# Kernel tuning notes

Measured on AMD Instinct MI355X. Metric: run time of the kernel, lower is better.

## Reference

```python
import jax, jax.numpy as jnp
import numpy as np

D_MODEL = 768
NUM_HEADS = 12
D_K = D_MODEL // NUM_HEADS
WINDOW = 16
SPARSITY = 0.8
NEG = -1e9


def _pos_encoding(seq_len, d_model, dtype):
    pos = jnp.arange(seq_len, dtype=jnp.float32)[:, None]
    div = jnp.exp(jnp.arange(0, d_model, 2, dtype=jnp.float32) * (-np.log(10000.0) / d_model))
    pe = jnp.zeros((seq_len, d_model), dtype=jnp.float32)
    pe = pe.at[:, 0::2].set(jnp.sin(pos * div))
    pe = pe.at[:, 1::2].set(jnp.cos(pos * div))
    return pe.astype(dtype)


def _layernorm(x, gamma, beta, eps=1e-5):
    mu = jnp.mean(x, axis=-1, keepdims=True)
    var = jnp.mean(jnp.square(x - mu), axis=-1, keepdims=True)
    return (x - mu) * jax.lax.rsqrt(var + eps) * gamma + beta


def _split_heads(x):  # [B,S,D] -> [B,H,S,dk]
    b, s, _ = x.shape
    return x.reshape(b, s, NUM_HEADS, D_K).transpose(0, 2, 1, 3)


def _attn(q, k, v, mask):  # mask broadcastable to [B,H,S,S], bool
    scores = jnp.einsum('bhqd,bhkd->bhqk', q, k) / jnp.sqrt(jnp.asarray(D_K, q.dtype))
    scores = jnp.where(mask, scores, jnp.asarray(NEG, q.dtype))
    w = jax.nn.softmax(scores, axis=-1)
    out = jnp.einsum('bhqk,bhkd->bhqd', w, v)
    b, h, s, d = out.shape
    return out.transpose(0, 2, 1, 3).reshape(b, s, h * d)


def setup_inputs() -> dict:
    key = jax.random.key(0)
    ks = jax.random.split(key, 16)
    d = D_MODEL
    sc = 1.0 / np.sqrt(d)
    inp = {
        'x': jax.random.normal(ks[0], (2, 2048, d), jnp.float32),
        'wgq': jax.random.normal(ks[1], (d, d), jnp.float32) * sc,
        'wgk': jax.random.normal(ks[2], (d, d), jnp.float32) * sc,
        'wgv': jax.random.normal(ks[3], (d, d), jnp.float32) * sc,
        'wlq': jax.random.normal(ks[4], (d, d), jnp.float32) * sc,
        'wlk': jax.random.normal(ks[5], (d, d), jnp.float32) * sc,
        'wlv': jax.random.normal(ks[6], (d, d), jnp.float32) * sc,
        'wtq': jax.random.normal(ks[7], (d, d), jnp.float32) * sc,
        'wtk': jax.random.normal(ks[8], (d, d), jnp.float32) * sc,
        'wtv': jax.random.normal(ks[9], (d, d), jnp.float32) * sc,
        'w_out': jax.random.normal(ks[10], (3 * d, d), jnp.float32) * (1.0 / np.sqrt(3 * d)),
        'b_out': jnp.zeros((d,), jnp.float32),
        'w_gate': jax.random.normal(ks[11], (d, 3), jnp.float32) * sc,
        'b_gate': jnp.zeros((3,), jnp.float32),
        'w_sparse': jax.random.normal(ks[12], (d, 1), jnp.float32) * sc,
        'b_sparse': jnp.zeros((1,), jnp.float32),
        'g_gamma': jnp.ones((d,), jnp.float32), 'g_beta': jnp.zeros((d,), jnp.float32),
        'l_gamma': jnp.ones((d,), jnp.float32), 'l_beta': jnp.zeros((d,), jnp.float32),
        't_gamma': jnp.ones((d,), jnp.float32), 't_beta': jnp.zeros((d,), jnp.float32),
    }
    return inp


def reference(x, wgq, wgk, wgv, wlq, wlk, wlv, wtq, wtk, wtv,
              w_out, b_out, w_gate, b_gate, w_sparse, b_sparse,
              g_gamma, g_beta, l_gamma, l_beta, t_gamma, t_beta):
    b, s, d = x.shape
    # positional encoding branch input (dropout is identity at eval)
    x_pos = x + _pos_encoding(s, d, x.dtype)[None]

    # focus gate over mean-pooled tokens -> [B,3]
    fw = jax.nn.softmax(x.mean(axis=1) @ w_gate + b_gate, axis=-1)
    gw, lw, tw = fw[:, 0, None, None], fw[:, 1, None, None], fw[:, 2, None, None]

    # sparse (global) mask: keep top-k important columns per batch
    importance = (x @ w_sparse + b_sparse)[..., 0]  # [B,S]
    k = max(1, int((1.0 - SPARSITY) * s))
    _, topk_idx = jax.lax.top_k(importance, k)
    sparse = jnp.zeros((b, s), bool).at[jnp.arange(b)[:, None], topk_idx].set(True)
    sparse_mask = sparse[:, None, None, :]  # [B,1,1,S]

    idx = jnp.arange(s)
    rel = idx[None, :] - idx[:, None]
    half = WINDOW // 2
    local_mask = ((rel >= -half) & (rel <= half))[None, None]  # [1,1,S,S]

    stride = max(1, s // 8)
    temporal_cols = (idx % stride) == 0
    temporal_mask = jnp.broadcast_to(temporal_cols[None, :], (s, s))[None, None]

    # global branch
    g = _attn(_split_heads(x @ wgq), _split_heads(x @ wgk), _split_heads(x @ wgv), sparse_mask)
    g = _layernorm(g, g_gamma, g_beta)
    # local branch
    l = _attn(_split_heads(x @ wlq), _split_heads(x @ wlk), _split_heads(x @ wlv), local_mask)
    l = _layernorm(l, l_gamma, l_beta)
    # temporal branch (uses pos-encoded input)
    t = _attn(_split_heads(x_pos @ wtq), _split_heads(x_pos @ wtk), _split_heads(x_pos @ wtv), temporal_mask)
    t = _layernorm(t, t_gamma, t_beta)

    combined = jnp.concatenate([g * gw, l * lw, t * tw], axis=-1)
    return combined @ w_out + b_out
```

## Files before the change

### kernel.cpp

```cpp
#include <hip/hip_runtime.h>
#include <cstdint>

constexpr int BB   = 2;
constexpr int SS   = 2048;
constexpr int DD   = 768;
constexpr int HH   = 12;
constexpr int NTOK = BB * SS;
constexpr int KSEL = 409;
constexpr int KPAD = 448;
constexpr int NKT  = 7;

typedef __bf16 bf16x8 __attribute__((ext_vector_type(8)));
typedef float  f32x4  __attribute__((ext_vector_type(4)));

__device__ __forceinline__ float b2f(unsigned short u) {
  return __uint_as_float(((unsigned)u) << 16);
}
__device__ __forceinline__ unsigned short f2b(float f) {
  unsigned u = __float_as_uint(f);
  u += 0x7fffu + ((u >> 16) & 1u);
  return (unsigned short)(u >> 16);
}
__device__ __forceinline__ unsigned long long shfl_xor_u64(unsigned long long v, int m) {
  unsigned lo = (unsigned)v, hi = (unsigned)(v >> 32);
  lo = __shfl_xor(lo, m, 64);
  hi = __shfl_xor(hi, m, 64);
  return ((unsigned long long)hi << 32) | lo;
}

__device__ __forceinline__ void gload_lds16(const void* gsrc, void* ldst) {
  __builtin_amdgcn_global_load_lds(
      (__attribute__((address_space(1))) void*)(gsrc),
      (__attribute__((address_space(3))) void*)(ldst), 16, 0, 0);
}

__global__ __launch_bounds__(256) void mega_pre(
    const float* __restrict__ x, const float* __restrict__ wsp,
    const float* __restrict__ bsp,
    unsigned short* __restrict__ xb, unsigned short* __restrict__ xpb,
    float* __restrict__ imp,
    const float* w0, const float* w1, const float* w2, const float* w3,
    const float* w4, const float* w5, const float* w6, const float* w7,
    const float* w8, const float* w9,
    unsigned short* __restrict__ WTx4, unsigned short* __restrict__ WTkv,
    unsigned short* __restrict__ WTqt, unsigned short* __restrict__ WTtkv,
    unsigned short* __restrict__ WTo,
    float* __restrict__ partial) {
  __shared__ float tile[32][33];
  int id = blockIdx.x;
  int tid = threadIdx.x;

  if (id < SS) {
    int srow = id;
    const float* xr0 = x + (long)srow * DD;
    const float* xr1 = x + (long)(SS + srow) * DD;
    float acc0 = 0.f, acc1 = 0.f;
#pragma unroll
    for (int k = 0; k < 3; ++k) {
      int c = tid + k * 256;
      int j2 = c & ~1;
      float freq = __expf((float)j2 * -0.011992630692677323f);
      float ang = (float)srow * freq;
      float pe = (c & 1) ? cosf(ang) : sinf(ang);
      float w = wsp[c];
      float x0 = xr0[c], x1 = xr1[c];
      xb[(long)srow * DD + c]        = f2b(x0);
      xb[(long)(SS + srow) * DD + c] = f2b(x1);
      xpb[(long)srow * DD + c]        = f2b(x0 + pe);
      xpb[(long)(SS + srow) * DD + c] = f2b(x1 + pe);
      acc0 += x0 * w;
      acc1 += x1 * w;
    }
#pragma unroll
    for (int m = 1; m < 64; m <<= 1) {
      acc0 += __shfl_xor(acc0, m, 64);
      acc1 += __shfl_xor(acc1, m, 64);
    }
    __shared__ float red[8];
    int wv = tid >> 6, lane = tid & 63;
    if (lane == 0) { red[wv] = acc0; red[4 + wv] = acc1; }
    __syncthreads();
    if (tid == 0) {
      imp[srow]      = red[0] + red[1] + red[2] + red[3] + bsp[0];
      imp[SS + srow] = red[4] + red[5] + red[6] + red[7] + bsp[0];
    }
  } else if (id < SS + 6912) {
    int tidx = id - SS;
    int z, bx, by;
    if (tidx < 5184) { z = tidx / 576; int rem = tidx % 576; by = rem / 24; bx = rem % 24; }
    else             { z = 9; int rem = tidx - 5184; by = rem / 24; bx = rem % 24; }
    const float* srcs[10] = {w0, w1, w2, w3, w4, w5, w6, w7, w8, w9};
    const float* src = srcs[z];
    unsigned short* dst;
    int R = DD;
    switch (z) {
      case 0: dst = WTx4;                       break;
      case 1: dst = WTkv;                       break;
      case 2: dst = WTkv + (long)DD * DD;       break;
      case 3: dst = WTx4 + (long)DD * DD;       break;
      case 4: dst = WTx4 + (long)2 * DD * DD;   break;
      case 5: dst = WTx4 + (long)3 * DD * DD;   break;
      case 6: dst = WTqt;                       break;
      case 7: dst = WTtkv;                      break;
      case 8: dst = WTtkv + (long)DD * DD;      break;
      default: dst = WTo; R = 2304;             break;
    }
    int r0 = by * 32, c0 = bx * 32;
    int tx = tid & 31, ty = tid >> 5;
    for (int i = ty; i < 32; i += 8) tile[i][tx] = src[(long)(r0 + i) * DD + c0 + tx];
    __syncthreads();
    for (int i = ty; i < 32; i += 8) dst[(long)(c0 + i) * R + r0 + tx] = f2b(tile[tx][i]);
  } else {
    int rem = id - SS - 6912;
    int chunk = rem & 15, b = rem >> 4;
    for (int c = tid; c < DD; c += 256) {
      const float* xp = x + ((long)(b * SS + chunk * 128)) * DD + c;
      float acc = 0.f;
      for (int s2 = 0; s2 < 128; ++s2) acc += xp[(long)s2 * DD];
      partial[(long)(b * 16 + chunk) * DD + c] = acc;
    }
  }
}

__global__ __launch_bounds__(1024) void topk_gate2(
    const float* __restrict__ imp, int* __restrict__ sel,
    const float* __restrict__ partial, const float* __restrict__ w_gate,
    const float* __restrict__ b_gate, float* __restrict__ fw) {
  int tid = threadIdx.x;
  if (blockIdx.x < 2) {
    __shared__ unsigned long long keys[SS];
    int b = blockIdx.x;
    for (int i = tid; i < SS; i += 1024) {
      float v = imp[b * SS + i];
      unsigned u = __float_as_uint(v);
      u = (u & 0x80000000u) ? ~u : (u | 0x80000000u);
      unsigned du = ~u;
      keys[i] = ((unsigned long long)du << 32) | (unsigned)i;
    }
    __syncthreads();
    for (int k = 2; k <= SS; k <<= 1) {
      for (int j = k >> 1; j >= 64; j >>= 1) {
        for (int i = tid; i < SS; i += 1024) {
          int p = i ^ j;
          if (p > i) {
            unsigned long long a = keys[i], bb = keys[p];
            bool up = ((i & k) == 0);
            if ((a > bb) == up) { keys[i] = bb; keys[p] = a; }
          }
        }
        __syncthreads();
      }
      unsigned long long k0 = keys[tid], k1 = keys[tid + 1024];
      bool up0 = ((tid & k) == 0);
      bool up1 = (((tid + 1024) & k) == 0);
      int j0 = (k >> 1) < 32 ? (k >> 1) : 32;
      for (int j = j0; j >= 1; j >>= 1) {
        bool low = ((tid & j) == 0);
        unsigned long long p0 = shfl_xor_u64(k0, j);
        k0 = ((low == up0) == (k0 < p0)) ? k0 : p0;
        unsigned long long p1 = shfl_xor_u64(k1, j);
        k1 = ((low == up1) == (k1 < p1)) ? k1 : p1;
      }
      keys[tid] = k0; keys[tid + 1024] = k1;
      __syncthreads();
    }
    for (int i = tid; i < KSEL; i += 1024) sel[b * KSEL + i] = (int)(keys[i] & 0xffffffffu);
  } else {
    __shared__ float meanbuf[DD];
    __shared__ float lg[3];
    int b = blockIdx.x - 2;
    if (tid < DD) {
      float acc = 0.f;
      for (int p = 0; p < 16; ++p) acc += partial[(long)(b * 16 + p) * DD + tid];
      meanbuf[tid] = acc * (1.0f / (float)SS);
    }
    __syncthreads();
    if (tid < 3) {
      float acc = b_gate[tid];
      for (int d = 0; d < DD; ++d) acc += meanbuf[d] * w_gate[d * 3 + tid];
      lg[tid] = acc;
    }
    __syncthreads();
    if (tid == 0) {
      float mx = fmaxf(lg[0], fmaxf(lg[1], lg[2]));
      float e0 = expf(lg[0] - mx), e1 = expf(lg[1] - mx), e2 = expf(lg[2] - mx);
      float inv = 1.f / (e0 + e1 + e2);
      fw[b * 3 + 0] = e0 * inv; fw[b * 3 + 1] = e1 * inv; fw[b * 3 + 2] = e2 * inv;
    }
  }
}

__global__ __launch_bounds__(256) void gemm_multi(
    const unsigned short* __restrict__ xb,    const unsigned short* __restrict__ WTx4,
    unsigned short* __restrict__ QKV4,
    const unsigned short* __restrict__ WTkv,  unsigned short* __restrict__ KVg,
    const unsigned short* __restrict__ xpb,   const unsigned short* __restrict__ WTqt,
    unsigned short* __restrict__ Qt,
    const unsigned short* __restrict__ WTtkv,
    const int* __restrict__ sel,
    unsigned short* __restrict__ K8, unsigned short* __restrict__ Vt8,
    unsigned short* __restrict__ Vt, unsigned short* __restrict__ Vtl) {
  __shared__ unsigned short AsB[2][4096];
  __shared__ unsigned short BsB[2][4096];
  constexpr int K = DD;
  const int tid = threadIdx.x;
  const int lane = tid & 63;
  const int wv = tid >> 6;
  const int wr = wv >> 1, wc = wv & 1;

  int lin = blockIdx.x;
  int swz = (lin & 7) * 132 + (lin >> 3);
  const unsigned short* BT;
  int ntx, tile, region;
  if (swz < 768)       { BT = WTx4;  ntx = 24; tile = swz;        region = 0; }
  else if (swz < 852)  { BT = WTkv;  ntx = 12; tile = swz - 768;  region = 1; }
  else if (swz < 1044) { BT = WTqt;  ntx = 6;  tile = swz - 852;  region = 2; }
  else                 { BT = WTtkv; ntx = 12; tile = swz - 1044; region = 3; }
  const long rowBase = (long)(tile / ntx) * 128;
  const long colBase = (long)(tile % ntx) * 128;

  auto arow = [&](int r) -> const unsigned short* {
    long grow = rowBase + r;
    if (region == 0) return xb + grow * (long)K;
    if (region == 2) return xpb + grow * (long)K;
    if (region == 1) {
      int bb2 = (int)(grow / KPAD), j = (int)(grow % KPAD);
      int srow = (j < KSEL) ? sel[bb2 * KSEL + j] : 0;
      return xb + ((long)bb2 * SS + srow) * (long)K;
    }
    if (grow < 16) {
      int bb2 = (int)grow >> 3, j = ((int)grow & 7) * 256;
      return xpb + ((long)bb2 * SS + j) * (long)K;
    }
    return xpb;
  };

  f32x4 acc[4][4];
#pragma unroll
  for (int i = 0; i < 4; ++i)
#pragma unroll
    for (int j = 0; j < 4; ++j)
#pragma unroll
      for (int r = 0; r < 4; ++r) acc[i][j][r] = 0.f;

  const int g0 = tid, g1 = tid + 256;
  const int r0 = g0 >> 2, k80 = (g0 & 3) ^ ((r0 >> 1) & 3);
  const int r1 = g1 >> 2, k81 = (g1 & 3) ^ ((r1 >> 1) & 3);
  const unsigned short* ga0 = arow(r0) + k80 * 8;
  const unsigned short* ga1 = arow(r1) + k81 * 8;
  const unsigned short* gb0 = BT + (colBase + r0) * (long)K + k80 * 8;
  const unsigned short* gb1 = BT + (colBase + r1) * (long)K + k81 * 8;

  const int k8 = lane >> 4;
  const int fr = lane & 15;
  int aoff[4], boff[4];
#pragma unroll
  for (int i = 0; i < 4; ++i) {
    int rowA = wr * 64 + i * 16 + fr;
    aoff[i] = (rowA * 4 + (k8 ^ ((rowA >> 1) & 3))) * 8;
    int rowB = wc * 64 + i * 16 + fr;
    boff[i] = (rowB * 4 + (k8 ^ ((rowB >> 1) & 3))) * 8;
  }

  auto stage = [&](int buf, int t) {
    int ko = t * 32;
    gload_lds16(ga0 + ko, &AsB[buf][g0 * 8]);
    gload_lds16(ga1 + ko, &AsB[buf][g1 * 8]);
    gload_lds16(gb0 + ko, &BsB[buf][g0 * 8]);
    gload_lds16(gb1 + ko, &BsB[buf][g1 * 8]);
  };

  constexpr int nk = K >> 5;
  stage(0, 0);
  __syncthreads();
  for (int t = 0; t < nk; ++t) {
    int cur = t & 1;
    if (t + 1 < nk) stage(cur ^ 1, t + 1);
    bf16x8 af[4], bfr[4];
#pragma unroll
    for (int i = 0; i < 4; ++i) af[i] = *(const bf16x8*)(&AsB[cur][aoff[i]]);
#pragma unroll
    for (int i = 0; i < 4; ++i) bfr[i] = *(const bf16x8*)(&BsB[cur][boff[i]]);
#pragma unroll
    for (int mi = 0; mi < 4; ++mi)
#pragma unroll
      for (int ni = 0; ni < 4; ++ni)
        acc[mi][ni] = __builtin_amdgcn_mfma_f32_16x16x32_bf16(af[mi], bfr[ni], acc[mi][ni], 0, 0, 0);
    __syncthreads();
  }

  int mode, vcol0 = 0, N = 0;
  unsigned short* C = nullptr;
  if (region == 0)      { mode = (colBase >= 2304) ? 1 : 0; C = QKV4; N = 3072;
                          vcol0 = (int)colBase - 2304; }
  else if (region == 1) { mode = (colBase >= 768) ? 2 : 0;  C = KVg;  N = 1536;
                          vcol0 = (int)colBase - 768; }
  else if (region == 2) { mode = 0; C = Qt; N = 768; }
  else                  { mode = (colBase >= 768) ? 4 : 3;
                          vcol0 = (int)colBase - 768; }

  const int orow0 = (lane >> 4) * 4;
  if (mode == 0) {
#pragma unroll
    for (int mi = 0; mi < 4; ++mi) {
      long gr = rowBase + wr * 64 + mi * 16 + orow0;
#pragma unroll
      for (int ni = 0; ni < 4; ++ni) {
        long gc = colBase + wc * 64 + ni * 16 + fr;
#pragma unroll
        for (int r = 0; r < 4; ++r)
          C[(gr + r) * (long)N + gc] = f2b(acc[mi][ni][r]);
      }
    }
  } else {
#pragma unroll
    for (int mi = 0; mi < 4; ++mi) {
      int lr = wr * 64 + mi * 16 + orow0;
      int grow = (int)rowBase + lr;
#pragma unroll
      for (int ni = 0; ni < 4; ++ni) {
        int lc = wc * 64 + ni * 16 + fr;
        uint2 pk;
        pk.x = (unsigned)f2b(acc[mi][ni][0]) | ((unsigned)f2b(acc[mi][ni][1]) << 16);
        pk.y = (unsigned)f2b(acc[mi][ni][2]) | ((unsigned)f2b(acc[mi][ni][3]) << 16);
        if (mode == 1) {
          int bb2 = grow >> 11, s = grow & (SS - 1);
          *(uint2*)(Vtl + ((long)bb2 * DD + vcol0 + lc) * SS + s) = pk;
        } else if (mode == 2) {
          int bb2 = grow / KPAD, j = grow - bb2 * KPAD;
          *(uint2*)(Vt + ((long)bb2 * DD + vcol0 + lc) * KPAD + j) = pk;
        } else if (mode == 3) {
          if (grow < 16) {
#pragma unroll
            for (int r = 0; r < 4; ++r) {
              int g2 = grow + r;
              K8[((long)(g2 >> 3) * 16 + (g2 & 7)) * DD + colBase + lc] =
                  f2b(acc[mi][ni][r]);
            }
          }
        } else {
          if (grow < 16) {
            *(uint2*)(Vt8 + ((long)(grow >> 3) * DD + vcol0 + lc) * 32 + (grow & 7)) = pk;
          }
        }
      }
    }
    if (mode == 3) {
      int row16 = tid >> 4, cg = tid & 15;
      int bb2 = row16 >> 3, jj = 8 + (row16 & 7);
      uint4 z4 = {0u, 0u, 0u, 0u};
      *(uint4*)(K8 + ((long)bb2 * 16 + jj) * DD + colBase + cg * 8) = z4;
    }
    if (mode == 4) {
#pragma unroll
      for (int e = 0; e < 6; ++e) {
        int id = tid + e * 256;
        int bb2 = id / 768, rem = id % 768;
        int c = rem / 6, ch = rem % 6;
        *(uint2*)(Vt8 + ((long)bb2 * DD + vcol0 + c) * 32 + 8 + ch * 4) = uint2{0u, 0u};
      }
    }
  }
}

__global__ __launch_bounds__(256) void gemm_final_sk(const unsigned short* __restrict__ A,
                                                     const unsigned short* __restrict__ BT,
                                                     float* __restrict__ Cpart) {
  __shared__ unsigned short As[2][128 * 32];
  __shared__ unsigned short Bs[2][128 * 32];
  constexpr int N = 768, K = 2304, CK = 768;
  const int tid = threadIdx.x;
  const int lane = tid & 63;
  const int wv = tid >> 6;
  const int wr = wv >> 1, wc = wv & 1;
  const int z = blockIdx.z;

  int lin = blockIdx.y * gridDim.x + blockIdx.x;
  int swz = (lin & 7) * 24 + (lin >> 3);
  const long rowBase = (long)(swz / 6) * 128;
  const long colBase = (long)(swz % 6) * 128;

  f32x4 acc[4][4];
#pragma unroll
  for (int i = 0; i < 4; ++i)
#pragma unroll
    for (int j = 0; j < 4; ++j)
#pragma unroll
      for (int r = 0; r < 4; ++r) acc[i][j][r] = 0.f;

  const int g0 = tid, g1 = tid + 256;
  const int r0 = g0 >> 2, k80 = (g0 & 3) ^ ((r0 >> 1) & 3);
  const int r1 = g1 >> 2, k81 = (g1 & 3) ^ ((r1 >> 1) & 3);
  const unsigned short* ga0 = A + (rowBase + r0) * (long)K + z * CK + k80 * 8;
  const unsigned short* ga1 = A + (rowBase + r1) * (long)K + z * CK + k81 * 8;
  const unsigned short* gb0 = BT + (colBase + r0) * (long)K + z * CK + k80 * 8;
  const unsigned short* gb1 = BT + (colBase + r1) * (long)K + z * CK + k81 * 8;

  const int k8 = lane >> 4;
  const int fr = lane & 15;
  int aoff[4], boff[4];
#pragma unroll
  for (int i = 0; i < 4; ++i) {
    int rowA = wr * 64 + i * 16 + fr;
    aoff[i] = (rowA * 4 + (k8 ^ ((rowA >> 1) & 3))) * 8;
    int rowB = wc * 64 + i * 16 + fr;
    boff[i] = (rowB * 4 + (k8 ^ ((rowB >> 1) & 3))) * 8;
  }

  auto stage = [&](int buf, int t) {
    int ko = t * 32;
    gload_lds16(ga0 + ko, &As[buf][g0 * 8]);
    gload_lds16(ga1 + ko, &As[buf][g1 * 8]);
    gload_lds16(gb0 + ko, &Bs[buf][g0 * 8]);
    gload_lds16(gb1 + ko, &Bs[buf][g1 * 8]);
  };

  constexpr int nk = CK >> 5;
  stage(0, 0);
  __syncthreads();
  for (int t = 0; t < nk; ++t) {
    int cur = t & 1;
    if (t + 1 < nk) stage(cur ^ 1, t + 1);
    bf16x8 af[4], bfr[4];
#pragma unroll
    for (int i = 0; i < 4; ++i) af[i] = *(const bf16x8*)(&As[cur][aoff[i]]);
#pragma unroll
    for (int i = 0; i < 4; ++i) bfr[i] = *(const bf16x8*)(&Bs[cur][boff[i]]);
#pragma unroll
    for (int mi = 0; mi < 4; ++mi)
#pragma unroll
      for (int ni = 0; ni < 4; ++ni)
        acc[mi][ni] = __builtin_amdgcn_mfma_f32_16x16x32_bf16(af[mi], bfr[ni], acc[mi][ni], 0, 0, 0);
    __syncthreads();
  }

  float* Cz = Cpart + (long)z * NTOK * DD;
  const int orow0 = (lane >> 4) * 4;
#pragma unroll
  for (int mi = 0; mi < 4; ++mi) {
    long gr = rowBase + wr * 64 + mi * 16 + orow0;
#pragma unroll
    for (int ni = 0; ni < 4; ++ni) {
      long gc = colBase + wc * 64 + ni * 16 + fr;
#pragma unroll
      for (int r = 0; r < 4; ++r)
        Cz[(gr + r) * (long)N + gc] = acc[mi][ni][r];
    }
  }
}

__global__ __launch_bounds__(256) void reduce_out(const float* __restrict__ P,
                                                  const float* __restrict__ bias,
                                                  float* __restrict__ out) {
  long i = (long)blockIdx.x * 256 + threadIdx.x;
  const f32x4* p0 = (const f32x4*)P;
  const f32x4* p1 = (const f32x4*)(P + (long)NTOK * DD);
  const f32x4* p2 = (const f32x4*)(P + 2L * NTOK * DD);
  f32x4 v = p0[i];
  v += p1[i];
  v += p2[i];
  int c4 = (int)(i % (DD / 4));
  v += *(const f32x4*)(bias + c4 * 4);
  ((f32x4*)out)[i] = v;
}

__device__ __forceinline__ void attn_flash_body(
    const unsigned short* __restrict__ QKV4,
    const unsigned short* __restrict__ KVg,
    const unsigned short* __restrict__ Vt,
    unsigned short* __restrict__ comb,
    unsigned short* smem) {
  unsigned short* Kl = smem;
  unsigned short* Vl = smem + 8192;
  unsigned short* Pl = smem + 16384;
  int tid = threadIdx.x, w = tid >> 6, lane = tid & 63;
  int fr = lane & 15, g = lane >> 4;
  int b = blockIdx.y / HH, h = blockIdx.y % HH, hoff = h * 64;
  int qbase = blockIdx.x * 64 + w * 16;
  long qrow = (long)b * SS + qbase + fr;

  const unsigned short* qptr = QKV4 + qrow * 3072 + hoff + g * 8;
  bf16x8 bq0 = *(const bf16x8*)(qptr);
  bf16x8 bq1 = *(const bf16x8*)(qptr + 32);

  const int s0 = tid, s1 = tid + 256;
  const int r0 = s0 >> 3, c0 = (s0 & 7) ^ (r0 & 7);
  const int r1 = s1 >> 3, c1 = (s1 & 7) ^ (r1 & 7);
  const unsigned short* kg_b = KVg + (long)b * KPAD * 1536 + hoff;
  const unsigned short* vt_b = Vt + ((long)b * DD + hoff) * KPAD;

  auto stage = [&](int buf, int t0) {
    gload_lds16(kg_b + (long)(t0 * 64 + r0) * 1536 + c0 * 8, &Kl[buf * 4096 + s0 * 8]);
    gload_lds16(kg_b + (long)(t0 * 64 + r1) * 1536 + c1 * 8, &Kl[buf * 4096 + s1 * 8]);
    gload_lds16(vt_b + (long)r0 * KPAD + t0 * 64 + c0 * 8, &Vl[buf * 4096 + s0 * 8]);
    gload_lds16(vt_b + (long)r1 * KPAD + t0 * 64 + c1 * 8, &Vl[buf * 4096 + s1 * 8]);
  };

  f32x4 oacc[4];
#pragma unroll
  for (int mf = 0; mf < 4; ++mf)
#pragma unroll
    for (int r = 0; r < 4; ++r) oacc[mf][r] = 0.f;
  float m = -3.0e38f, l = 0.f;

  stage(0, 0);
  asm volatile("s_waitcnt vmcnt(0)" ::: "memory");
  __syncthreads();

  for (int t = 0; t < NKT; ++t) {
    int cur = t & 1;
    if (t + 1 < NKT) stage(cur ^ 1, t + 1);

    f32x4 st[4];
#pragma unroll
    for (int kt = 0; kt < 4; ++kt) {
      int row = kt * 16 + fr;
      bf16x8 a0 = *(const bf16x8*)(&Kl[cur * 4096 + (row * 8 + (g ^ (row & 7))) * 8]);
      bf16x8 a1 = *(const bf16x8*)(&Kl[cur * 4096 + (row * 8 + ((4 + g) ^ (row & 7))) * 8]);
      f32x4 z = {0.f, 0.f, 0.f, 0.f};
      z = __builtin_amdgcn_mfma_f32_16x16x32_bf16(a0, bq0, z, 0, 0, 0);
      st[kt] = __builtin_amdgcn_mfma_f32_16x16x32_bf16(a1, bq1, z, 0, 0, 0);
    }

    float tm = -3.0e38f;
#pragma unroll
    for (int kt = 0; kt < 4; ++kt)
#pragma unroll
      for (int r = 0; r < 4; ++r) {
        int key = t * 64 + kt * 16 + g * 4 + r;
        float s = (key < KSEL) ? st[kt][r] * 0.125f : -1.0e30f;
        st[kt][r] = s;
        tm = fmaxf(tm, s);
      }
    tm = fmaxf(tm, __shfl_xor(tm, 16, 64));
    tm = fmaxf(tm, __shfl_xor(tm, 32, 64));
    float newm = fmaxf(m, tm);
    float f = __expf(m - newm);
    float tsum = 0.f;
#pragma unroll
    for (int kt = 0; kt < 4; ++kt)
#pragma unroll
      for (int r = 0; r < 4; ++r) {
        float e = __expf(st[kt][r] - newm);
        st[kt][r] = e;
        tsum += e;
      }
    tsum += __shfl_xor(tsum, 16, 64);
    tsum += __shfl_xor(tsum, 32, 64);
    l = l * f + tsum;
    m = newm;
#pragma unroll
    for (int mf = 0; mf < 4; ++mf)
#pragma unroll
      for (int r = 0; r < 4; ++r) oacc[mf][r] *= f;

    unsigned short* pw = &Pl[w * 1088 + fr * 68 + g * 4];
#pragma unroll
    for (int kt = 0; kt < 4; ++kt) {
      uint2 pk;
      pk.x = (unsigned)f2b(st[kt][0]) | ((unsigned)f2b(st[kt][1]) << 16);
      pk.y = (unsigned)f2b(st[kt][2]) | ((unsigned)f2b(st[kt][3]) << 16);
      *(uint2*)(pw + kt * 16) = pk;
    }

    const unsigned short* prd = &Pl[w * 1088 + fr * 68];
#pragma unroll
    for (int ks2 = 0; ks2 < 2; ++ks2) {
      bf16x8 pf = *(const bf16x8*)(prd + ks2 * 32 + g * 8);
#pragma unroll
      for (int mf = 0; mf < 4; ++mf) {
        int vr = mf * 16 + fr;
        int vc = ks2 * 4 + g;
        bf16x8 vf = *(const bf16x8*)(&Vl[cur * 4096 + (vr * 8 + (vc ^ (vr & 7))) * 8]);
        oacc[mf] = __builtin_amdgcn_mfma_f32_16x16x32_bf16(vf, pf, oacc[mf], 0, 0, 0);
      }
    }

    asm volatile("s_waitcnt vmcnt(0)" ::: "memory");
    __syncthreads();
  }

  float inv = 1.f / l;
  unsigned short* orow = comb + qrow * 2304 + hoff;
#pragma unroll
  for (int mf = 0; mf < 4; ++mf) {
    uint2 pk;
    pk.x = (unsigned)f2b(oacc[mf][0] * inv) | ((unsigned)f2b(oacc[mf][1] * inv) << 16);
    pk.y = (unsigned)f2b(oacc[mf][2] * inv) | ((unsigned)f2b(oacc[mf][3] * inv) << 16);
    *(uint2*)(orow + mf * 16 + g * 4) = pk;
  }
}

__device__ __forceinline__ void attn_win_body(
    const unsigned short* __restrict__ QKV,
    const unsigned short* __restrict__ K8,
    const unsigned short* __restrict__ Vt,
    unsigned short* __restrict__ comb, int brOff,
    int LD, int QO, long VSTR, bool local,
    unsigned short* smem) {
  int tid = threadIdx.x, w = tid >> 6, lane = tid & 63;
  int fr = lane & 15, g = lane >> 4;
  int b = blockIdx.y / HH, h = blockIdx.y % HH, hoff = h * 64;
  int qbase = blockIdx.x * 64 + w * 16;
  long qrow = (long)b * SS + qbase + fr;

  const unsigned short* qptr = QKV + qrow * LD + QO + hoff + g * 8;
  bf16x8 bq0 = *(const bf16x8*)(qptr);
  bf16x8 bq1 = *(const bf16x8*)(qptr + 32);

  int kstart = qbase - 8;
  if (kstart < 0) kstart = 0;
  if (kstart > SS - 32) kstart = SS - 32;

  f32x4 st[2];
  if (local) {
#pragma unroll
    for (int kt = 0; kt < 2; ++kt) {
      const unsigned short* kp =
          QKV + ((long)b * SS + kstart + kt * 16 + fr) * LD + 1536 + hoff + g * 8;
      bf16x8 a0 = *(const bf16x8*)(kp);
      bf16x8 a1 = *(const bf16x8*)(kp + 32);
      f32x4 z = {0.f, 0.f, 0.f, 0.f};
      z = __builtin_amdgcn_mfma_f32_16x16x32_bf16(a0, bq0, z, 0, 0, 0);
      st[kt] = __builtin_amdgcn_mfma_f32_16x16x32_bf16(a1, bq1, z, 0, 0, 0);
    }
  } else {
    const unsigned short* kp = K8 + ((long)b * 16 + fr) * DD + hoff + g * 8;
    bf16x8 a0 = *(const bf16x8*)(kp);
    bf16x8 a1 = *(const bf16x8*)(kp + 32);
    f32x4 z = {0.f, 0.f, 0.f, 0.f};
    z = __builtin_amdgcn_mfma_f32_16x16x32_bf16(a0, bq0, z, 0, 0, 0);
    st[0] = __builtin_amdgcn_mfma_f32_16x16x32_bf16(a1, bq1, z, 0, 0, 0);
    st[1] = f32x4{0.f, 0.f, 0.f, 0.f};
  }

  float m = -3.0e38f;
#pragma unroll
  for (int kt = 0; kt < 2; ++kt)
#pragma unroll
    for (int r = 0; r < 4; ++r) {
      int idx = kt * 16 + g * 4 + r;
      bool valid;
      if (local) {
        int rel = kstart + idx - qbase - fr;
        valid = (rel >= -8) && (rel <= 8);
      } else {
        valid = (idx < 8);
      }
      float s = valid ? st[kt][r] * 0.125f : -1.0e30f;
      st[kt][r] = s;
      m = fmaxf(m, s);
    }
  m = fmaxf(m, __shfl_xor(m, 16, 64));
  m = fmaxf(m, __shfl_xor(m, 32, 64));

  float lsum = 0.f;
#pragma unroll
  for (int kt = 0; kt < 2; ++kt)
#pragma unroll
    for (int r = 0; r < 4; ++r) {
      float e = __expf(st[kt][r] - m);
      st[kt][r] = e;
      lsum += e;
    }
  lsum += __shfl_xor(lsum, 16, 64);
  lsum += __shfl_xor(lsum, 32, 64);

  unsigned short* pl = smem + w * 640 + fr * 40 + g * 4;
#pragma unroll
  for (int kt = 0; kt < 2; ++kt) {
    uint2 pk;
    pk.x = (unsigned)f2b(st[kt][0]) | ((unsigned)f2b(st[kt][1]) << 16);
    pk.y = (unsigned)f2b(st[kt][2]) | ((unsigned)f2b(st[kt][3]) << 16);
    *(uint2*)(pl + kt * 16) = pk;
  }

  f32x4 oacc[4];
#pragma unroll
  for (int mf = 0; mf < 4; ++mf)
#pragma unroll
    for (int r = 0; r < 4; ++r) oacc[mf][r] = 0.f;

  const unsigned short* pr = smem + w * 640 + fr * 40 + g * 8;
  bf16x8 pf = *(const bf16x8*)(pr);
  long kb2 = local ? kstart : 0;
#pragma unroll
  for (int mf = 0; mf < 4; ++mf) {
    const unsigned short* vp =
        Vt + ((long)b * DD + hoff + mf * 16 + fr) * VSTR + kb2 + g * 8;
    bf16x8 vf = *(const bf16x8*)(vp);
    oacc[mf] = __builtin_amdgcn_mfma_f32_16x16x32_bf16(vf, pf, oacc[mf], 0, 0, 0);
  }

  float inv = 1.f / lsum;
  unsigned short* orow = comb + qrow * 2304 + brOff + hoff;
#pragma unroll
  for (int mf = 0; mf < 4; ++mf) {
    uint2 pk;
    pk.x = (unsigned)f2b(oacc[mf][0] * inv) | ((unsigned)f2b(oacc[mf][1] * inv) << 16);
    pk.y = (unsigned)f2b(oacc[mf][2] * inv) | ((unsigned)f2b(oacc[mf][3] * inv) << 16);
    *(uint2*)(orow + mf * 16 + g * 4) = pk;
  }
}

__global__ __launch_bounds__(256) void attn_all(
    const unsigned short* __restrict__ QKV4,
    const unsigned short* __restrict__ KVg,
    const unsigned short* __restrict__ Vt,
    const unsigned short* __restrict__ Qt,
    const unsigned short* __restrict__ K8,
    const unsigned short* __restrict__ Vt8,
    const unsigned short* __restrict__ Vtl,
    unsigned short* __restrict__ comb) {
  __shared__ unsigned short smem[20736];
  int z = blockIdx.z;
  if (z == 0) {
    attn_flash_body(QKV4, KVg, Vt, comb, smem);
  } else if (z == 1) {
    attn_win_body(QKV4, nullptr, Vtl, comb, 768, 3072, 768, SS, true, smem);
  } else {
    attn_win_body(Qt, K8, Vt8, comb, 1536, 768, 0, 32, false, smem);
  }
}

__global__ __launch_bounds__(256) void ln_gate_inplace(
    unsigned short* __restrict__ comb,
    const float* __restrict__ gg, const float* __restrict__ gb,
    const float* __restrict__ lgam, const float* __restrict__ lbet,
    const float* __restrict__ tg, const float* __restrict__ tb,
    const float* __restrict__ fw) {
  int row = blockIdx.x;
  int b = row >> 11;
  int tid = threadIdx.x;
  __shared__ float red[8];
  const float* gams[3] = {gg, lgam, tg};
  const float* bets[3] = {gb, lbet, tb};
#pragma unroll
  for (int br = 0; br < 3; ++br) {
    unsigned short* p = comb + (long)row * 2304 + br * DD;
    float x0 = b2f(p[tid]), x1 = b2f(p[tid + 256]), x2 = b2f(p[tid + 512]);
    float s = x0 + x1 + x2;
    float ss = x0 * x0 + x1 * x1 + x2 * x2;
#pragma unroll
    for (int msk = 1; msk < 64; msk <<= 1) {
      s += __shfl_xor(s, msk, 64);
      ss += __shfl_xor(ss, msk, 64);
    }
    int wv = tid >> 6, lane = tid & 63;
    if (lane == 0) { red[wv] = s; red[4 + wv] = ss; }
    __syncthreads();
    float S4 = red[0] + red[1] + red[2] + red[3];
    float SQ = red[4] + red[5] + red[6] + red[7];
    float mean = S4 * (1.f / (float)DD);
    float var = SQ * (1.f / (float)DD) - mean * mean;
    float rs = rsqrtf(var + 1e-5f);
    float gate = fw[b * 3 + br];
    const float* gam = gams[br];
    const float* bet = bets[br];
    p[tid]       = f2b(((x0 - mean) * rs * gam[tid]       + bet[tid])       * gate);
    p[tid + 256] = f2b(((x1 - mean) * rs * gam[tid + 256] + bet[tid + 256]) * gate);
    p[tid + 512] = f2b(((x2 - mean) * rs * gam[tid + 512] + bet[tid + 512]) * gate);
    __syncthreads();
  }
}

extern "C" void kernel_launch(void* const* d_in, const int* in_sizes, int n_in,
                              void* d_out, int out_size, void* d_ws, size_t ws_size,
                              hipStream_t stream) {
  const float* x        = (const float*)d_in[0];
  const float* wgq      = (const float*)d_in[1];
  const float* wgk      = (const float*)d_in[2];
  const float* wgv      = (const float*)d_in[3];
  const float* wlq      = (const float*)d_in[4];
  const float* wlk      = (const float*)d_in[5];
  const float* wlv      = (const float*)d_in[6];
  const float* wtq      = (const float*)d_in[7];
  const float* wtk      = (const float*)d_in[8];
  const float* wtv      = (const float*)d_in[9];
  const float* w_out    = (const float*)d_in[10];
  const float* b_out    = (const float*)d_in[11];
  const float* w_gate   = (const float*)d_in[12];
  const float* b_gate   = (const float*)d_in[13];
  const float* w_sparse = (const float*)d_in[14];
  const float* b_sparse = (const float*)d_in[15];
  const float* g_gamma  = (const float*)d_in[16];
  const float* g_beta   = (const float*)d_in[17];
  const float* l_gamma  = (const float*)d_in[18];
  const float* l_beta   = (const float*)d_in[19];
  const float* t_gamma  = (const float*)d_in[20];
  const float* t_beta   = (const float*)d_in[21];
  float* outp = (float*)d_out;

  unsigned short* xb    = (unsigned short*)d_ws;
  unsigned short* xpb   = xb    + (long)NTOK * DD;
  unsigned short* WTx4  = xpb   + (long)NTOK * DD;
  unsigned short* WTkv  = WTx4  + (long)3072 * DD;
  unsigned short* WTqt  = WTkv  + (long)1536 * DD;
  unsigned short* WTtkv = WTqt  + (long)DD * DD;
  unsigned short* WTo   = WTtkv + (long)1536 * DD;
  unsigned short* QKV4  = WTo   + (long)DD * 2304;
  unsigned short* Qt    = QKV4  + (long)NTOK * 3072;
  unsigned short* KVg   = Qt    + (long)NTOK * DD;
  unsigned short* K8    = KVg   + (long)BB * KPAD * 1536;
  unsigned short* Vt8   = K8    + (long)BB * 16 * DD;
  unsigned short* Vt    = Vt8   + (long)BB * DD * 32;
  unsigned short* Vtl   = Vt    + (long)BB * DD * KPAD;
  unsigned short* comb  = Vtl   + (long)BB * DD * SS;
  float* Cpart   = (float*)(comb + (long)NTOK * 2304);
  float* imp     = Cpart + 3L * NTOK * DD;
  float* partial = imp + NTOK;
  float* fw      = partial + 32 * DD;
  int*   sel     = (int*)(fw + 8);

  mega_pre<<<SS + 6912 + 32, 256, 0, stream>>>(
      x, w_sparse, b_sparse, xb, xpb, imp,
      wgq, wgk, wgv, wlq, wlk, wlv, wtq, wtk, wtv, w_out,
      WTx4, WTkv, WTqt, WTtkv, WTo, partial);
  topk_gate2<<<4, 1024, 0, stream>>>(imp, sel, partial, w_gate, b_gate, fw);

  gemm_multi<<<1056, 256, 0, stream>>>(xb, WTx4, QKV4, WTkv, KVg,
                                       xpb, WTqt, Qt, WTtkv, sel,
                                       K8, Vt8, Vt, Vtl);

  attn_all<<<dim3(32, BB * HH, 3), 256, 0, stream>>>(QKV4, KVg, Vt, Qt, K8, Vt8,
                                                     Vtl, comb);

  ln_gate_inplace<<<NTOK, 256, 0, stream>>>(comb, g_gamma, g_beta,
                                            l_gamma, l_beta, t_gamma, t_beta, fw);
  gemm_final_sk<<<dim3(6, 32, 3), 256, 0, stream>>>(comb, WTo, Cpart);
  reduce_out<<<NTOK * DD / 4 / 256, 256, 0, stream>>>(Cpart, b_out, outp);
}
```

Baseline: 172.0 us.

## Fuse split-K reduction into final GEMM via atomics and remap QKV tile swizzle

Replaces the three split-K partial buffers and the separate reduce_out kernel with float atomicAdd straight into the zero-initialised output, adding the bias only from the z==0 slice. This removes a full partial-sum write and read pass plus one kernel launch, at the cost of an extra memset and atomic traffic. The result also becomes non-deterministic in summation order. Separately, the projection GEMM's block-to-tile mapping is changed so each XCD gets a contiguous 16x6 patch of QKV tiles for better L2 reuse. The zero-fill of the K8 padding rows is dropped, presumably relying on masking or on prior contents.

```diff
diff --git a/kernel.cpp b/kernel.cpp
--- a/kernel.cpp
+++ b/kernel.cpp
@@ -209,13 +209,20 @@
   const int wr = wv >> 1, wc = wv & 1;
 
   int lin = blockIdx.x;
-  int swz = (lin & 7) * 132 + (lin >> 3);
+  int xcd = lin & 7, idx = lin >> 3;
   const unsigned short* BT;
   int ntx, tile, region;
-  if (swz < 768)       { BT = WTx4;  ntx = 24; tile = swz;        region = 0; }
-  else if (swz < 852)  { BT = WTkv;  ntx = 12; tile = swz - 768;  region = 1; }
-  else if (swz < 1044) { BT = WTqt;  ntx = 6;  tile = swz - 852;  region = 2; }
-  else                 { BT = WTtkv; ntx = 12; tile = swz - 1044; region = 3; }
+  if (idx < 96) {
+    region = 0; BT = WTx4; ntx = 24;
+    int r = (xcd >> 2) * 16 + (idx & 15);
+    int c = (xcd & 3) * 6 + (idx >> 4);
+    tile = r * 24 + c;
+  } else {
+    int e = xcd * 36 + (idx - 96);
+    if (e < 84)       { region = 1; BT = WTkv;  ntx = 12; tile = e; }
+    else if (e < 276) { region = 2; BT = WTqt;  ntx = 6;  tile = e - 84; }
+    else              { region = 3; BT = WTtkv; ntx = 12; tile = e - 276; }
+  }
   const long rowBase = (long)(tile / ntx) * 128;
   const long colBase = (long)(tile % ntx) * 128;
 
@@ -345,12 +352,6 @@
         }
       }
     }
-    if (mode == 3) {
-      int row16 = tid >> 4, cg = tid & 15;
-      int bb2 = row16 >> 3, jj = 8 + (row16 & 7);
-      uint4 z4 = {0u, 0u, 0u, 0u};
-      *(uint4*)(K8 + ((long)bb2 * 16 + jj) * DD + colBase + cg * 8) = z4;
-    }
     if (mode == 4) {
 #pragma unroll
       for (int e = 0; e < 6; ++e) {
@@ -365,7 +366,8 @@
 
 __global__ __launch_bounds__(256) void gemm_final_sk(const unsigned short* __restrict__ A,
                                                      const unsigned short* __restrict__ BT,
-                                                     float* __restrict__ Cpart) {
+                                                     const float* __restrict__ bias,
+                                                     float* __restrict__ out) {
   __shared__ unsigned short As[2][128 * 32];
   __shared__ unsigned short Bs[2][128 * 32];
   constexpr int N = 768, K = 2304, CK = 768;
@@ -434,7 +436,6 @@
     __syncthreads();
   }
 
-  float* Cz = Cpart + (long)z * NTOK * DD;
   const int orow0 = (lane >> 4) * 4;
 #pragma unroll
   for (int mi = 0; mi < 4; ++mi) {
@@ -442,26 +443,12 @@
 #pragma unroll
     for (int ni = 0; ni < 4; ++ni) {
       long gc = colBase + wc * 64 + ni * 16 + fr;
+      float bv = (z == 0) ? bias[gc] : 0.f;
 #pragma unroll
       for (int r = 0; r < 4; ++r)
-        Cz[(gr + r) * (long)N + gc] = acc[mi][ni][r];
-    }
-  }
-}
-
-__global__ __launch_bounds__(256) void reduce_out(const float* __restrict__ P,
-                                                  const float* __restrict__ bias,
-                                                  float* __restrict__ out) {
-  long i = (long)blockIdx.x * 256 + threadIdx.x;
-  const f32x4* p0 = (const f32x4*)P;
-  const f32x4* p1 = (const f32x4*)(P + (long)NTOK * DD);
-  const f32x4* p2 = (const f32x4*)(P + 2L * NTOK * DD);
-  f32x4 v = p0[i];
-  v += p1[i];
-  v += p2[i];
-  int c4 = (int)(i % (DD / 4));
-  v += *(const f32x4*)(bias + c4 * 4);
-  ((f32x4*)out)[i] = v;
+        atomicAdd(&out[(gr + r) * (long)N + gc], acc[mi][ni][r] + bv);
+    }
+  }
 }
 
 __device__ __forceinline__ void attn_flash_body(
@@ -806,11 +793,12 @@
   unsigned short* Vt    = Vt8   + (long)BB * DD * 32;
   unsigned short* Vtl   = Vt    + (long)BB * DD * KPAD;
   unsigned short* comb  = Vtl   + (long)BB * DD * SS;
-  float* Cpart   = (float*)(comb + (long)NTOK * 2304);
-  float* imp     = Cpart + 3L * NTOK * DD;
+  float* imp     = (float*)(comb + (long)NTOK * 2304);
   float* partial = imp + NTOK;
   float* fw      = partial + 32 * DD;
   int*   sel     = (int*)(fw + 8);
+
+  hipMemsetAsync(outp, 0, (size_t)NTOK * DD * sizeof(float), stream);
 
   mega_pre<<<SS + 6912 + 32, 256, 0, stream>>>(
       x, w_sparse, b_sparse, xb, xpb, imp,
@@ -827,6 +815,5 @@
 
   ln_gate_inplace<<<NTOK, 256, 0, stream>>>(comb, g_gamma, g_beta,
                                             l_gamma, l_beta, t_gamma, t_beta, fw);
-  gemm_final_sk<<<dim3(6, 32, 3), 256, 0, stream>>>(comb, WTo, Cpart);
-  reduce_out<<<NTOK * DD / 4 / 256, 256, 0, stream>>>(Cpart, b_out, outp);
-}
+  gemm_final_sk<<<dim3(6, 32, 3), 256, 0, stream>>>(comb, WTo, b_out, outp);
+}
```

Result: slower. 190.7 us (+10.9%).
